# Performance work log

Measured on AMD Instinct MI355X. Metric: run time of the kernel, lower is better.

## Reference

```python
import jax, jax.numpy as jnp
import numpy as np

N_NODES = 50000
IN_C, HID, N_CLS = 128, 128, 16
N_EDGES = 800000


def gcn_conv(x, W, b, src, dst, deg_inv_sqrt, n_nodes):
    # PyG GCNConv: h = x @ W; out[dst] += norm * h[src]; out += b
    h = x @ W                                   # [N, out_c]
    norm = deg_inv_sqrt[src] * deg_inv_sqrt[dst]  # [E]
    msgs = h[src] * norm[:, None]               # gather + scale, [E, out_c]
    out = jax.ops.segment_sum(msgs, dst, num_segments=n_nodes)
    return out + b


def setup_inputs() -> dict:
    key = jax.random.key(0)
    k1, k2, k3, k4, k5 = jax.random.split(key, 5)
    x = jax.random.normal(k1, (N_NODES, IN_C), dtype=jnp.float32)
    edge_index = jax.random.randint(k2, (2, N_EDGES), 0, N_NODES, dtype=jnp.int64)
    # glorot-ish params (torch.manual_seed(1234) in source only affects init values)
    def lin(k, fan_in, fan_out):
        s = 1.0 / np.sqrt(fan_in)
        kw, kb = jax.random.split(k)
        W = jax.random.uniform(kw, (fan_in, fan_out), minval=-s, maxval=s, dtype=jnp.float32)
        b = jax.random.uniform(kb, (fan_out,), minval=-s, maxval=s, dtype=jnp.float32)
        return W, b
    W1, b1 = lin(k3, IN_C, HID)
    W2, b2 = lin(k4, HID, HID)
    Wh, bh = lin(k5, HID, N_CLS)
    return {"x": x, "edge_index": edge_index, "W1": W1, "b1": b1,
            "W2": W2, "b2": b2, "Wh": Wh, "bh": bh}


def reference(x, edge_index, W1, b1, W2, b2, Wh, bh):
    n = x.shape[0]
    # add self-loops (PyG GCNConv default add_self_loops=True)
    loops = jnp.arange(n, dtype=edge_index.dtype)
    src = jnp.concatenate([edge_index[0], loops])
    dst = jnp.concatenate([edge_index[1], loops])
    # symmetric normalization D^{-1/2} (A+I) D^{-1/2}; degree over dst with unit weights
    deg = jax.ops.segment_sum(jnp.ones(src.shape[0], dtype=x.dtype), dst, num_segments=n)
    dis = jnp.where(deg > 0, jax.lax.rsqrt(deg), 0.0)
    h = gcn_conv(x, W1, b1, src, dst, dis, n)
    h = jax.nn.relu(h)
    h = gcn_conv(h, W2, b2, src, dst, dis, n)
    h = jax.nn.relu(h)
    return h @ Wh + bh
```

## Files before the change

### kernel.cpp

```cpp
#include <hip/hip_runtime.h>

#define CH 128
#define NCLS 16
#define CHK 32
#define NCHUNK 4
#define ECAP 131072

typedef __attribute__((ext_vector_type(8))) short bf16x8;
typedef __attribute__((ext_vector_type(4))) float f32x4;
typedef __attribute__((ext_vector_type(8))) _Float16 f16x8;

__device__ inline ushort f2bf(float f) {
    unsigned u = __float_as_uint(f);
    unsigned r = u + 0x7fffu + ((u >> 16) & 1u);
    return (ushort)(r >> 16);
}
__device__ inline float bf2f(ushort b) {
    return __uint_as_float(((unsigned)b) << 16);
}
__device__ inline ushort f2h(float f) {
    _Float16 h = (_Float16)f;
    ushort u;
    __builtin_memcpy(&u, &h, 2);
    return u;
}

__global__ __launch_bounds__(256) void prep_kernel(
    const float* __restrict__ W1, const float* __restrict__ W2,
    ushort* __restrict__ w1hi, ushort* __restrict__ w1lo,
    ushort* __restrict__ w2hi, ushort* __restrict__ w2lo,
    int* __restrict__ cnt, int* __restrict__ pcnt, int* __restrict__ galloc,
    ushort* __restrict__ hC, int n, int nbz) {
    int b = blockIdx.x, tid = threadIdx.x;
    if (b < 128) {
        const float* W = (b < 64) ? W1 : W2;
        ushort* Whi = (b < 64) ? w1hi : w2hi;
        ushort* Wlo = (b < 64) ? w1lo : w2lo;
        int t = ((b & 63) << 8) + tid;
        int k = t >> 7, nn = t & 127;
        float v = W[t];
        ushort h = f2bf(v);
        Whi[nn * CH + k] = h;
        Wlo[nn * CH + k] = f2bf(v - bf2f(h));
    } else if (b < 128 + nbz) {
        int i = (b - 128) * 256 + tid;
        if (i < n) cnt[i] = 0;
    } else {
        if (tid < NCHUNK * CHK) {
            int c = tid >> 5, ch = tid & 31;
            hC[((size_t)c * (n + 1) + n) * CHK + ch] = 0;
        }
        if (tid < 8) pcnt[tid] = 0;
        if (tid == 8) *galloc = 0;
    }
}

__global__ __launch_bounds__(256) void bucketcount_kernel(
    const int* __restrict__ src, const int* __restrict__ dst,
    unsigned* __restrict__ ebuf, int* __restrict__ pcnt,
    int* __restrict__ cnt, int E, float p8n) {
    __shared__ int lpos[8];
    __shared__ int lbase[8];
    int tid = threadIdx.x;
    if (tid < 8) lpos[tid] = 0;
    __syncthreads();
    int i0 = (blockIdx.x * 256 + tid) * 4;
    int part[4]; int off[4]; unsigned pk[4]; int c = 0;
    if (i0 + 3 < E) {
        int4 s4 = *(const int4*)&src[i0];
        int4 d4 = *(const int4*)&dst[i0];
        int ss[4] = {s4.x, s4.y, s4.z, s4.w};
        int dd[4] = {d4.x, d4.y, d4.z, d4.w};
        c = 4;
#pragma unroll
        for (int k = 0; k < 4; k++) {
            part[k] = min(7, (int)((float)dd[k] * p8n));
            pk[k] = ((unsigned)dd[k] << 16) | (unsigned)ss[k];
            off[k] = atomicAdd(&lpos[part[k]], 1);
            atomicAdd(&cnt[dd[k]], 1);
        }
    } else {
        for (int k = 0; k < 4 && i0 + k < E; k++) {
            int s = src[i0 + k], d = dst[i0 + k];
            part[c] = min(7, (int)((float)d * p8n));
            pk[c] = ((unsigned)d << 16) | (unsigned)s;
            off[c] = atomicAdd(&lpos[part[c]], 1);
            atomicAdd(&cnt[d], 1);
            c++;
        }
    }
    __syncthreads();
    if (tid < 8) lbase[tid] = atomicAdd(&pcnt[tid], lpos[tid]);
    __syncthreads();
    for (int k = 0; k < c; k++) {
        int idx = lbase[part[k]] + off[k];
        if (idx < ECAP) ebuf[(size_t)part[k] * ECAP + idx] = pk[k];
    }
}

__global__ __launch_bounds__(256) void place_kernel(
    const int* __restrict__ cnt, int* __restrict__ rsp,
    int* __restrict__ cursor, int* __restrict__ galloc,
    ushort* __restrict__ esrc, int n) {
    __shared__ int lds[256];
    __shared__ int gbase;
    int t = threadIdx.x;
    int i = blockIdx.x * 256 + t;
    int c = (i < n) ? cnt[i] : 0;
    int sz = (i < n) ? ((c + 8) & ~7) : 0;
    lds[t] = sz;
    __syncthreads();
    for (int off = 1; off < 256; off <<= 1) {
        int x = (t >= off) ? lds[t - off] : 0;
        __syncthreads();
        lds[t] += x;
        __syncthreads();
    }
    int incl = lds[t];
    if (t == 255) gbase = atomicAdd(galloc, incl);
    __syncthreads();
    int base = gbase + incl - sz;
    if (i < n) {
        rsp[i] = base;
        cursor[i] = base + 1;
        esrc[base] = (ushort)i;
        for (int p = base + 1 + c; p < base + sz; p++) esrc[p] = (ushort)n;
    }
}

template <bool RELU_IN>
__device__ __forceinline__ void gemm_body(
    int bx, int by, const float* __restrict__ A,
    const ushort* __restrict__ Bthi, const ushort* __restrict__ Btlo,
    const int* __restrict__ cntp, ushort* __restrict__ C16, int n_rows) {
    const int tid = threadIdx.x;
    const int bm0 = bx * 128;
    const int wv = tid >> 6;
    const int lane = tid & 63;
    const int col = lane & 15;
    const int quad = lane >> 4;
    const int rbase = bm0 + wv * 32 + col;
    const int ntBase = by * 4;

    f32x4 acc[2][4];
#pragma unroll
    for (int m = 0; m < 2; m++)
#pragma unroll
        for (int t = 0; t < 4; t++) acc[m][t] = (f32x4){0.f, 0.f, 0.f, 0.f};

#pragma unroll
    for (int k0 = 0; k0 < 4; k0++) {
        const int kb = k0 * 32 + quad * 8;
        bf16x8 ah[2], al[2];
#pragma unroll
        for (int m = 0; m < 2; m++) {
            int arow = rbase + m * 16;
            bool av = (arow < n_rows);
            const float* __restrict__ Ap = A + (size_t)arow * CH + kb;
            float4 f0 = av ? *(const float4*)Ap       : make_float4(0.f, 0.f, 0.f, 0.f);
            float4 f1 = av ? *(const float4*)(Ap + 4) : make_float4(0.f, 0.f, 0.f, 0.f);
            if (RELU_IN) {
                f0.x = fmaxf(f0.x, 0.f); f0.y = fmaxf(f0.y, 0.f);
                f0.z = fmaxf(f0.z, 0.f); f0.w = fmaxf(f0.w, 0.f);
                f1.x = fmaxf(f1.x, 0.f); f1.y = fmaxf(f1.y, 0.f);
                f1.z = fmaxf(f1.z, 0.f); f1.w = fmaxf(f1.w, 0.f);
            }
            float fa[8] = {f0.x, f0.y, f0.z, f0.w, f1.x, f1.y, f1.z, f1.w};
#pragma unroll
            for (int j = 0; j < 8; j++) {
                ushort h = f2bf(fa[j]);
                ah[m][j] = (short)h;
                al[m][j] = (short)f2bf(fa[j] - bf2f(h));
            }
        }
#pragma unroll
        for (int t = 0; t < 4; t++) {
            const int boff = ((ntBase + t) * 16 + col) * CH + kb;
            bf16x8 bh = *(const bf16x8*)&Bthi[boff];
            bf16x8 bl = *(const bf16x8*)&Btlo[boff];
#pragma unroll
            for (int m = 0; m < 2; m++) {
                acc[m][t] = __builtin_amdgcn_mfma_f32_16x16x32_bf16(ah[m], bh, acc[m][t], 0, 0, 0);
                acc[m][t] = __builtin_amdgcn_mfma_f32_16x16x32_bf16(ah[m], bl, acc[m][t], 0, 0, 0);
                acc[m][t] = __builtin_amdgcn_mfma_f32_16x16x32_bf16(al[m], bh, acc[m][t], 0, 0, 0);
            }
        }
    }

#pragma unroll
    for (int m = 0; m < 2; m++) {
#pragma unroll
        for (int reg = 0; reg < 4; reg++) {
            int gr = bm0 + wv * 32 + m * 16 + quad * 4 + reg;
            if (gr < n_rows) {
                float d = rsqrtf((float)cntp[gr] + 1.0f);
#pragma unroll
                for (int tp = 0; tp < 4; tp += 2) {
                    int nt0 = ntBase + tp;
                    int chunk = nt0 >> 1;
                    unsigned h0 = f2h(acc[m][tp][reg] * d);
                    unsigned h1 = f2h(acc[m][tp + 1][reg] * d);
                    unsigned pk = h0 | (h1 << 16);
                    __builtin_nontemporal_store(pk,
                        (unsigned*)&C16[((size_t)chunk * (n_rows + 1) + gr) * CHK
                                        + 2 * col]);
                }
            }
        }
    }
}

template <bool RELU_IN>
__global__ __launch_bounds__(256, 4) void gemmfill_kernel(
    const float* __restrict__ A, const ushort* __restrict__ Bthi,
    const ushort* __restrict__ Btlo, const int* __restrict__ cntp,
    ushort* __restrict__ C16, int n_rows, int nbx, int gemmBlocks,
    const unsigned* __restrict__ ebuf, const int* __restrict__ pcnt,
    int* __restrict__ cursor, ushort* __restrict__ esrc) {
    int b = blockIdx.x;
    if (b < gemmBlocks) {
        gemm_body<RELU_IN>(b % nbx, b / nbx, A, Bthi, Btlo, cntp, C16, n_rows);
    } else {
        int fb = b - gemmBlocks;
        int part = fb & 7;
        int m = min(pcnt[part], ECAP);
        const unsigned* bk = ebuf + (size_t)part * ECAP;
        for (int e = (fb >> 3) * 256 + (int)threadIdx.x; e < m; e += 256 * 256) {
            unsigned pe = bk[e];
            int p = atomicAdd(&cursor[pe >> 16], 1);
            esrc[p] = (ushort)(pe & 0xffffu);
        }
    }
}

__global__ __launch_bounds__(256) void gather_kernel(
    const int* __restrict__ rsp, const int* __restrict__ cnt,
    const ushort* __restrict__ esrc, const ushort* __restrict__ hC16,
    const float* __restrict__ bias, float* __restrict__ out, int n) {
    int c = blockIdx.x & 3;
    int bic = blockIdx.x >> 2;
    int wv = threadIdx.x >> 6;
    int lane = threadIdx.x & 63;
    int g = lane >> 2;
    int q = lane & 3;
    int i = bic * 64 + wv * 16 + g;
    bool valid = (i < n);
    int iw = valid ? i : 0;
    const f16x8* __restrict__ h8 = (const f16x8*)(hC16 + (size_t)c * (n + 1) * CHK);

    float warm = 0.f;
    {
        int nbr = (n + 63) >> 6;
        const float4* __restrict__ w4 = (const float4*)h8;
        size_t p = (size_t)bic * 256 + threadIdx.x;
        size_t sliceF4 = ((size_t)(n + 1) * CHK) >> 3;
        for (; p < sliceF4; p += (size_t)nbr * 256) {
            float4 v = w4[p];
            warm += v.x + v.y + v.z + v.w;
        }
    }

    int beg = valid ? rsp[iw] : 0;
    int cv  = valid ? cnt[iw] : -8;
    int pc  = (cv + 8) & ~7;
    float accA[4] = {0.f, 0.f, 0.f, 0.f};
    float accB[4] = {0.f, 0.f, 0.f, 0.f};
    for (int j = beg; j < beg + pc; j += 8) {
        ushort4 e0 = *(const ushort4*)&esrc[j];
        ushort4 e1 = *(const ushort4*)&esrc[j + 4];
        f16x8 v0 = h8[(size_t)e0.x * 4 + q];
        f16x8 v1 = h8[(size_t)e0.y * 4 + q];
        f16x8 v2 = h8[(size_t)e0.z * 4 + q];
        f16x8 v3 = h8[(size_t)e0.w * 4 + q];
        f16x8 v4 = h8[(size_t)e1.x * 4 + q];
        f16x8 v5 = h8[(size_t)e1.y * 4 + q];
        f16x8 v6 = h8[(size_t)e1.z * 4 + q];
        f16x8 v7 = h8[(size_t)e1.w * 4 + q];
#pragma unroll
        for (int s = 0; s < 4; s++) {
            accA[s] += (float)v0[2 * s]; accB[s] += (float)v0[2 * s + 1];
            accA[s] += (float)v1[2 * s]; accB[s] += (float)v1[2 * s + 1];
            accA[s] += (float)v2[2 * s]; accB[s] += (float)v2[2 * s + 1];
            accA[s] += (float)v3[2 * s]; accB[s] += (float)v3[2 * s + 1];
            accA[s] += (float)v4[2 * s]; accB[s] += (float)v4[2 * s + 1];
            accA[s] += (float)v5[2 * s]; accB[s] += (float)v5[2 * s + 1];
            accA[s] += (float)v6[2 * s]; accB[s] += (float)v6[2 * s + 1];
            accA[s] += (float)v7[2 * s]; accB[s] += (float)v7[2 * s + 1];
        }
    }
    __asm__ volatile("" : : "v"(warm));
    if (valid) {
        float di = rsqrtf((float)cv + 1.0f);
        const float4* bias4 = (const float4*)bias;
        float4 bvA = bias4[8 * c + q];
        float4 bvB = bias4[8 * c + 4 + q];
        f32x4 oA, oB;
        oA[0] = bvA.x + di * accA[0]; oA[1] = bvA.y + di * accA[1];
        oA[2] = bvA.z + di * accA[2]; oA[3] = bvA.w + di * accA[3];
        oB[0] = bvB.x + di * accB[0]; oB[1] = bvB.y + di * accB[1];
        oB[2] = bvB.z + di * accB[2]; oB[3] = bvB.w + di * accB[3];
        float4* out4 = (float4*)out;
        __builtin_nontemporal_store(oA, (f32x4*)&out4[(size_t)iw * 32 + 8 * c + q]);
        __builtin_nontemporal_store(oB, (f32x4*)&out4[(size_t)iw * 32 + 8 * c + 4 + q]);
    }
}

__global__ __launch_bounds__(256) void head_kernel(
    const float* __restrict__ A, const float* __restrict__ Wh,
    const float* __restrict__ bh, float* __restrict__ out, int n) {
    __shared__ float Ws[CH * NCLS];
    __shared__ float As[16][129];
    const int tid = threadIdx.x;
    const int n0 = blockIdx.x * 16;
#pragma unroll
    for (int i = 0; i < 8; i++) {
        int l = tid + i * 256;
        Ws[l] = Wh[l];
    }
#pragma unroll
    for (int i = 0; i < 8; i++) {
        int l = tid + i * 256;
        int r = l >> 7, c = l & 127;
        int gr = n0 + r;
        As[r][c] = (gr < n) ? fmaxf(A[(size_t)gr * CH + c], 0.0f) : 0.0f;
    }
    __syncthreads();
    int r = tid >> 4, c = tid & 15;
    float acc = bh[c];
#pragma unroll
    for (int k = 0; k < CH; k++) acc = fmaf(As[r][k], Ws[k * NCLS + c], acc);
    int gr = n0 + r;
    if (gr < n) out[(size_t)gr * NCLS + c] = acc;
}

extern "C" void kernel_launch(void* const* d_in, const int* in_sizes, int n_in,
                              void* d_out, int out_size, void* d_ws, size_t ws_size,
                              hipStream_t stream) {
    const float* x  = (const float*)d_in[0];
    const int*   ei = (const int*)d_in[1];
    const float* W1 = (const float*)d_in[2];
    const float* b1 = (const float*)d_in[3];
    const float* W2 = (const float*)d_in[4];
    const float* b2 = (const float*)d_in[5];
    const float* Wh = (const float*)d_in[6];
    const float* bh = (const float*)d_in[7];
    float* out = (float*)d_out;

    const int n = in_sizes[0] / CH;
    const int E = in_sizes[1] / 2;
    const int* src = ei;
    const int* dst = ei + E;

    ushort* w1hi = (ushort*)d_ws;
    ushort* w1lo = w1hi + CH * CH;
    ushort* w2hi = w1lo + CH * CH;
    ushort* w2lo = w2hi + CH * CH;
    ushort* hA  = w2lo + CH * CH;
    float* bufB = (float*)(hA + (size_t)(n + 1) * CH);
    int* cnt    = (int*)(bufB + (size_t)n * CH);
    int* rsp    = cnt + n;
    int* cursor = rsp + n;
    int* pcnt   = cursor + n;
    int* galloc = pcnt + 8;
    ushort* esrc = (ushort*)(pcnt + 16);
    unsigned* ebuf = (unsigned*)bufB;

    const int B = 256;
    const int nbz = (n + B - 1) / B;
    const int nbx = (n + 127) / 128;
    const int gemmBlocks = nbx * 2;
    const int nbr = (n + 63) / 64;
    const int gatherGrid = NCHUNK * nbr;
    const float p8n = 8.0f / (float)n;

    prep_kernel<<<128 + nbz + 1, B, 0, stream>>>(W1, W2, w1hi, w1lo, w2hi, w2lo,
                                                 cnt, pcnt, galloc, hA, n, nbz);
    bucketcount_kernel<<<(E + 1023) / 1024, B, 0, stream>>>(src, dst, ebuf, pcnt,
                                                            cnt, E, p8n);
    place_kernel<<<nbz, B, 0, stream>>>(cnt, rsp, cursor, galloc, esrc, n);

    gemmfill_kernel<false><<<gemmBlocks + 2048, B, 0, stream>>>(
        x, w1hi, w1lo, cnt, hA, n, nbx, gemmBlocks, ebuf, pcnt, cursor, esrc);
    gather_kernel<<<gatherGrid, B, 0, stream>>>(rsp, cnt, esrc, hA, b1, bufB, n);
    gemmfill_kernel<true><<<gemmBlocks, B, 0, stream>>>(
        bufB, w2hi, w2lo, cnt, hA, n, nbx, gemmBlocks, ebuf, pcnt, cursor, esrc);
    gather_kernel<<<gatherGrid, B, 0, stream>>>(rsp, cnt, esrc, hA, b2, bufB, n);
    head_kernel<<<(n + 15) / 16, B, 0, stream>>>(bufB, Wh, bh, out, n);
}
```

Baseline: 262.6 us.

## Store layer outputs as fp16 with fused ReLU and use fp16 MFMA for second GEMM

The gather kernel now applies ReLU and writes its output as fp16 instead of fp32, halving the intermediate write and read traffic. A dedicated second-layer GEMM reads those fp16 activations directly and uses fp16 MFMA with a hi/lo split of W2 only, so it issues two MFMAs per tile step where the old path did three bf16 ones and no longer converts the input. The head kernel reads the fp16 activations too. In exchange, hidden activations are rounded to fp16, which adds error and could overflow if values grow large.

```diff
diff --git a/kernel.cpp b/kernel.cpp
--- a/kernel.cpp
+++ b/kernel.cpp
@@ -9,6 +9,7 @@
 typedef __attribute__((ext_vector_type(8))) short bf16x8;
 typedef __attribute__((ext_vector_type(4))) float f32x4;
 typedef __attribute__((ext_vector_type(8))) _Float16 f16x8;
+typedef __attribute__((ext_vector_type(4))) ushort u16x4;
 
 __device__ inline ushort f2bf(float f) {
     unsigned u = __float_as_uint(f);
@@ -24,24 +25,33 @@
     __builtin_memcpy(&u, &h, 2);
     return u;
 }
+__device__ inline float h2f(ushort u) {
+    _Float16 h;
+    __builtin_memcpy(&h, &u, 2);
+    return (float)h;
+}
 
 __global__ __launch_bounds__(256) void prep_kernel(
     const float* __restrict__ W1, const float* __restrict__ W2,
     ushort* __restrict__ w1hi, ushort* __restrict__ w1lo,
-    ushort* __restrict__ w2hi, ushort* __restrict__ w2lo,
+    ushort* __restrict__ w2hf, ushort* __restrict__ w2lf,
     int* __restrict__ cnt, int* __restrict__ pcnt, int* __restrict__ galloc,
     ushort* __restrict__ hC, int n, int nbz) {
     int b = blockIdx.x, tid = threadIdx.x;
-    if (b < 128) {
-        const float* W = (b < 64) ? W1 : W2;
-        ushort* Whi = (b < 64) ? w1hi : w2hi;
-        ushort* Wlo = (b < 64) ? w1lo : w2lo;
-        int t = ((b & 63) << 8) + tid;
+    if (b < 64) {
+        int t = (b << 8) + tid;
         int k = t >> 7, nn = t & 127;
-        float v = W[t];
+        float v = W1[t];
         ushort h = f2bf(v);
-        Whi[nn * CH + k] = h;
-        Wlo[nn * CH + k] = f2bf(v - bf2f(h));
+        w1hi[nn * CH + k] = h;
+        w1lo[nn * CH + k] = f2bf(v - bf2f(h));
+    } else if (b < 128) {
+        int t = ((b - 64) << 8) + tid;
+        int k = t >> 7, nn = t & 127;
+        float v = W2[t];
+        ushort h = f2h(v);
+        w2hf[nn * CH + k] = h;
+        w2lf[nn * CH + k] = f2h(v - h2f(h));
     } else if (b < 128 + nbz) {
         int i = (b - 128) * 256 + tid;
         if (i < n) cnt[i] = 0;
@@ -128,8 +138,7 @@
     }
 }
 
-template <bool RELU_IN>
-__device__ __forceinline__ void gemm_body(
+__device__ __forceinline__ void gemm1_body(
     int bx, int by, const float* __restrict__ A,
     const ushort* __restrict__ Bthi, const ushort* __restrict__ Btlo,
     const int* __restrict__ cntp, ushort* __restrict__ C16, int n_rows) {
@@ -159,12 +168,6 @@
             const float* __restrict__ Ap = A + (size_t)arow * CH + kb;
             float4 f0 = av ? *(const float4*)Ap       : make_float4(0.f, 0.f, 0.f, 0.f);
             float4 f1 = av ? *(const float4*)(Ap + 4) : make_float4(0.f, 0.f, 0.f, 0.f);
-            if (RELU_IN) {
-                f0.x = fmaxf(f0.x, 0.f); f0.y = fmaxf(f0.y, 0.f);
-                f0.z = fmaxf(f0.z, 0.f); f0.w = fmaxf(f0.w, 0.f);
-                f1.x = fmaxf(f1.x, 0.f); f1.y = fmaxf(f1.y, 0.f);
-                f1.z = fmaxf(f1.z, 0.f); f1.w = fmaxf(f1.w, 0.f);
-            }
             float fa[8] = {f0.x, f0.y, f0.z, f0.w, f1.x, f1.y, f1.z, f1.w};
 #pragma unroll
             for (int j = 0; j < 8; j++) {
@@ -210,7 +213,6 @@
     }
 }
 
-template <bool RELU_IN>
 __global__ __launch_bounds__(256, 4) void gemmfill_kernel(
     const float* __restrict__ A, const ushort* __restrict__ Bthi,
     const ushort* __restrict__ Btlo, const int* __restrict__ cntp,
@@ -219,7 +221,7 @@
     int* __restrict__ cursor, ushort* __restrict__ esrc) {
     int b = blockIdx.x;
     if (b < gemmBlocks) {
-        gemm_body<RELU_IN>(b % nbx, b / nbx, A, Bthi, Btlo, cntp, C16, n_rows);
+        gemm1_body(b % nbx, b / nbx, A, Bthi, Btlo, cntp, C16, n_rows);
     } else {
         int fb = b - gemmBlocks;
         int part = fb & 7;
@@ -233,10 +235,76 @@
     }
 }
 
+__global__ __launch_bounds__(256, 4) void gemm2_kernel(
+    const ushort* __restrict__ A16, const ushort* __restrict__ Bhf,
+    const ushort* __restrict__ Blf, const int* __restrict__ cntp,
+    ushort* __restrict__ C16, int n_rows) {
+    const int tid = threadIdx.x;
+    const int bm0 = blockIdx.x * 128;
+    const int wv = tid >> 6;
+    const int lane = tid & 63;
+    const int col = lane & 15;
+    const int quad = lane >> 4;
+    const int rbase = bm0 + wv * 32 + col;
+    const int ntBase = blockIdx.y * 4;
+    const f16x8 fz = {0, 0, 0, 0, 0, 0, 0, 0};
+
+    f32x4 acc[2][4];
+#pragma unroll
+    for (int m = 0; m < 2; m++)
+#pragma unroll
+        for (int t = 0; t < 4; t++) acc[m][t] = (f32x4){0.f, 0.f, 0.f, 0.f};
+
+#pragma unroll
+    for (int k0 = 0; k0 < 4; k0++) {
+        const int kb = k0 * 32 + quad * 8;
+        f16x8 a[2];
+#pragma unroll
+        for (int m = 0; m < 2; m++) {
+            int arow = rbase + m * 16;
+            a[m] = (arow < n_rows)
+                 ? *(const f16x8*)(A16 + (size_t)arow * CH + kb) : fz;
+        }
+#pragma unroll
+        for (int t = 0; t < 4; t++) {
+            const int boff = ((ntBase + t) * 16 + col) * CH + kb;
+            f16x8 bh = *(const f16x8*)&Bhf[boff];
+            f16x8 bl = *(const f16x8*)&Blf[boff];
+#pragma unroll
+            for (int m = 0; m < 2; m++) {
+                acc[m][t] = __builtin_amdgcn_mfma_f32_16x16x32_f16(a[m], bh, acc[m][t], 0, 0, 0);
+                acc[m][t] = __builtin_amdgcn_mfma_f32_16x16x32_f16(a[m], bl, acc[m][t], 0, 0, 0);
+            }
+        }
+    }
+
+#pragma unroll
+    for (int m = 0; m < 2; m++) {
+#pragma unroll
+        for (int reg = 0; reg < 4; reg++) {
+            int gr = bm0 + wv * 32 + m * 16 + quad * 4 + reg;
+            if (gr < n_rows) {
+                float d = rsqrtf((float)cntp[gr] + 1.0f);
+#pragma unroll
+                for (int tp = 0; tp < 4; tp += 2) {
+                    int nt0 = ntBase + tp;
+                    int chunk = nt0 >> 1;
+                    unsigned h0 = f2h(acc[m][tp][reg] * d);
+                    unsigned h1 = f2h(acc[m][tp + 1][reg] * d);
+                    unsigned pk = h0 | (h1 << 16);
+                    __builtin_nontemporal_store(pk,
+                        (unsigned*)&C16[((size_t)chunk * (n_rows + 1) + gr) * CHK
+                                        + 2 * col]);
+                }
+            }
+        }
+    }
+}
+
 __global__ __launch_bounds__(256) void gather_kernel(
     const int* __restrict__ rsp, const int* __restrict__ cnt,
     const ushort* __restrict__ esrc, const ushort* __restrict__ hC16,
-    const float* __restrict__ bias, float* __restrict__ out, int n) {
+    const float* __restrict__ bias, ushort* __restrict__ out16, int n) {
     int c = blockIdx.x & 3;
     int bic = blockIdx.x >> 2;
     int wv = threadIdx.x >> 6;
@@ -294,19 +362,23 @@
         const float4* bias4 = (const float4*)bias;
         float4 bvA = bias4[8 * c + q];
         float4 bvB = bias4[8 * c + 4 + q];
-        f32x4 oA, oB;
-        oA[0] = bvA.x + di * accA[0]; oA[1] = bvA.y + di * accA[1];
-        oA[2] = bvA.z + di * accA[2]; oA[3] = bvA.w + di * accA[3];
-        oB[0] = bvB.x + di * accB[0]; oB[1] = bvB.y + di * accB[1];
-        oB[2] = bvB.z + di * accB[2]; oB[3] = bvB.w + di * accB[3];
-        float4* out4 = (float4*)out;
-        __builtin_nontemporal_store(oA, (f32x4*)&out4[(size_t)iw * 32 + 8 * c + q]);
-        __builtin_nontemporal_store(oB, (f32x4*)&out4[(size_t)iw * 32 + 8 * c + 4 + q]);
+        u16x4 pA, pB;
+        pA[0] = f2h(fmaxf(bvA.x + di * accA[0], 0.f));
+        pA[1] = f2h(fmaxf(bvA.y + di * accA[1], 0.f));
+        pA[2] = f2h(fmaxf(bvA.z + di * accA[2], 0.f));
+        pA[3] = f2h(fmaxf(bvA.w + di * accA[3], 0.f));
+        pB[0] = f2h(fmaxf(bvB.x + di * accB[0], 0.f));
+        pB[1] = f2h(fmaxf(bvB.y + di * accB[1], 0.f));
+        pB[2] = f2h(fmaxf(bvB.z + di * accB[2], 0.f));
+        pB[3] = f2h(fmaxf(bvB.w + di * accB[3], 0.f));
+        ushort* o16 = out16 + (size_t)iw * CH + 32 * c + 4 * q;
+        __builtin_nontemporal_store(pA, (u16x4*)o16);
+        __builtin_nontemporal_store(pB, (u16x4*)(o16 + 16));
     }
 }
 
 __global__ __launch_bounds__(256) void head_kernel(
-    const float* __restrict__ A, const float* __restrict__ Wh,
+    const ushort* __restrict__ A16, const float* __restrict__ Wh,
     const float* __restrict__ bh, float* __restrict__ out, int n) {
     __shared__ float Ws[CH * NCLS];
     __shared__ float As[16][129];
@@ -317,12 +389,13 @@
         int l = tid + i * 256;
         Ws[l] = Wh[l];
     }
-#pragma unroll
-    for (int i = 0; i < 8; i++) {
-        int l = tid + i * 256;
-        int r = l >> 7, c = l & 127;
-        int gr = n0 + r;
-        As[r][c] = (gr < n) ? fmaxf(A[(size_t)gr * CH + c], 0.0f) : 0.0f;
+    {
+        int row = tid >> 4, c0 = (tid & 15) * 8;
+        int gr = n0 + row;
+        const f16x8 fz = {0, 0, 0, 0, 0, 0, 0, 0};
+        f16x8 v = (gr < n) ? *(const f16x8*)(A16 + (size_t)gr * CH + c0) : fz;
+#pragma unroll
+        for (int j = 0; j < 8; j++) As[row][c0 + j] = fmaxf((float)v[j], 0.0f);
     }
     __syncthreads();
     int r = tid >> 4, c = tid & 15;
@@ -353,10 +426,10 @@
 
     ushort* w1hi = (ushort*)d_ws;
     ushort* w1lo = w1hi + CH * CH;
-    ushort* w2hi = w1lo + CH * CH;
-    ushort* w2lo = w2hi + CH * CH;
-    ushort* hA  = w2lo + CH * CH;
-    float* bufB = (float*)(hA + (size_t)(n + 1) * CH);
+    ushort* w2hf = w1lo + CH * CH;
+    ushort* w2lf = w2hf + CH * CH;
+    ushort* hA   = w2lf + CH * CH;
+    ushort* bufB = hA + (size_t)(n + 1) * CH;
     int* cnt    = (int*)(bufB + (size_t)n * CH);
     int* rsp    = cnt + n;
     int* cursor = rsp + n;
@@ -373,17 +446,16 @@
     const int gatherGrid = NCHUNK * nbr;
     const float p8n = 8.0f / (float)n;
 
-    prep_kernel<<<128 + nbz + 1, B, 0, stream>>>(W1, W2, w1hi, w1lo, w2hi, w2lo,
+    prep_kernel<<<128 + nbz + 1, B, 0, stream>>>(W1, W2, w1hi, w1lo, w2hf, w2lf,
                                                  cnt, pcnt, galloc, hA, n, nbz);
     bucketcount_kernel<<<(E + 1023) / 1024, B, 0, stream>>>(src, dst, ebuf, pcnt,
                                                             cnt, E, p8n);
     place_kernel<<<nbz, B, 0, stream>>>(cnt, rsp, cursor, galloc, esrc, n);
 
-    gemmfill_kernel<false><<<gemmBlocks + 2048, B, 0, stream>>>(
+    gemmfill_kernel<<<gemmBlocks + 2048, B, 0, stream>>>(
         x, w1hi, w1lo, cnt, hA, n, nbx, gemmBlocks, ebuf, pcnt, cursor, esrc);
     gather_kernel<<<gatherGrid, B, 0, stream>>>(rsp, cnt, esrc, hA, b1, bufB, n);
-    gemmfill_kernel<true><<<gemmBlocks, B, 0, stream>>>(
-        bufB, w2hi, w2lo, cnt, hA, n, nbx, gemmBlocks, ebuf, pcnt, cursor, esrc);
+    gemm2_kernel<<<dim3(nbx, 2), B, 0, stream>>>(bufB, w2hf, w2lf, cnt, hA, n);
     gather_kernel<<<gatherGrid, B, 0, stream>>>(rsp, cnt, esrc, hA, b2, bufB, n);
     head_kernel<<<(n + 15) / 16, B, 0, stream>>>(bufB, Wh, bh, out, n);
 }
```

Measured after the change: 254.1 us. -3.2%, faster.
